# Performance work log

Hardware: AMD Instinct MI355X
Metric: run time of the kernel (lower is better)

## Reference

```python
import jax, jax.numpy as jnp
import numpy as np

B, N, C = 2, 2048, 1024
H = 16
D = C // H  # head_dim = 64
SCALE = D ** -0.5


def setup_inputs() -> dict:
    key = jax.random.key(0)
    ks = jax.random.split(key, 9)
    s = C ** -0.5  # ~ torch Linear default init scale
    return {
        "x": jax.random.normal(ks[0], (B, N, C), dtype=jnp.float32),
        "Wq": jax.random.uniform(ks[1], (C, C), jnp.float32, -s, s),
        "bq": jax.random.uniform(ks[2], (C,), jnp.float32, -s, s),
        "Wk": jax.random.uniform(ks[3], (C, C), jnp.float32, -s, s),
        "bk": jax.random.uniform(ks[4], (C,), jnp.float32, -s, s),
        "Wv": jax.random.uniform(ks[5], (C, C), jnp.float32, -s, s),
        "bv": jax.random.uniform(ks[6], (C,), jnp.float32, -s, s),
        "Wo": jax.random.uniform(ks[7], (C, C), jnp.float32, -s, s),
        "bo": jax.random.uniform(ks[8], (C,), jnp.float32, -s, s),
    }


def reference(x, Wq, bq, Wk, bk, Wv, bv, Wo, bo):
    # Projections: [B,N,C] -> [B,H,N,D]
    def split_heads(t):
        return t.reshape(B, N, H, D).transpose(0, 2, 1, 3)

    q = split_heads(x @ Wq.T + bq)
    k = split_heads(x @ Wk.T + bk)
    v = split_heads(x @ Wv.T + bv)

    scores = jnp.einsum("bhnd,bhmd->bhnm", q, k) * SCALE  # [B,H,N,N]
    attn = jax.nn.softmax(scores, axis=-1)
    out = jnp.einsum("bhnm,bhmd->bhnd", attn, v)  # [B,H,N,D]
    out = out.transpose(0, 2, 1, 3).reshape(B, N, C)
    return out @ Wo.T + bo
```

## Files before the change

kernel.cpp:

```cpp
#include <hip/hip_runtime.h>
#include <stdint.h>


typedef _Float16 h8 __attribute__((ext_vector_type(8)));
typedef _Float16 h4 __attribute__((ext_vector_type(4)));
typedef float f4 __attribute__((ext_vector_type(4)));
typedef uint32_t u32;
typedef u32 u32x4 __attribute__((ext_vector_type(4)));

#define AS1(p) ((const __attribute__((address_space(1))) void*)(p))
#define AS3(p) ((__attribute__((address_space(3))) void*)(p))

template <int ITERS>
__device__ __forceinline__ void stage128B(const _Float16* g, int ldk, _Float16* s, int tid) {
#pragma unroll
  for (int j = 0; j < ITERS; ++j) {
    int off = j * 4096 + tid * 16;
    int row = off >> 7;
    int ch = (off >> 4) & 7;
    int gch = ch ^ (row & 7);
    __builtin_amdgcn_global_load_lds(AS1(g + row * ldk + gch * 8), AS3(s + (off >> 1)), 16, 0, 0);
  }
}

__device__ __forceinline__ void stage_k(const _Float16* g, _Float16* s, int tid) {
#pragma unroll
  for (int j = 0; j < 4; ++j) {
    int off = j * 4096 + tid * 16;
    int row = off >> 7;
    int ch = (off >> 4) & 7;
    int gch = ch ^ ((row >> 1) & 7);
    __builtin_amdgcn_global_load_lds(AS1(g + row * 64 + gch * 8), AS3(s + (off >> 1)), 16, 0, 0);
  }
}

__device__ __forceinline__ void stage_vt(const _Float16* g, _Float16* s, int tid) {
#pragma unroll
  for (int j = 0; j < 4; ++j) {
    int off = j * 4096 + tid * 16;
    int row = off >> 8;
    int ch = (off >> 4) & 15;
    int gch = ch ^ (row & 15);
    __builtin_amdgcn_global_load_lds(AS1(g + row * 2048 + gch * 8), AS3(s + (off >> 1)), 16, 0, 0);
  }
}

__device__ __forceinline__ h8 frag64(const _Float16* s, int row, int g) {
  return *(const h8*)(s + row * 64 + ((g ^ (row & 7)) << 3));
}
__device__ __forceinline__ h8 frag128(const _Float16* s, int row, int g) {
  return *(const h8*)(s + row * 128 + ((g ^ (row & 15)) << 3));
}

__global__ void cvt_all(const float* __restrict__ x, const float* __restrict__ Wq,
                        const float* __restrict__ Wk, const float* __restrict__ Wv,
                        const float* __restrict__ Wo, _Float16* __restrict__ xh,
                        _Float16* __restrict__ q, _Float16* __restrict__ k,
                        _Float16* __restrict__ v, _Float16* __restrict__ o) {
  int blk = blockIdx.x;
  const float* src; _Float16* dst; int off;
  if (blk < 4096)      { src = x;  dst = xh; off = blk; }
  else if (blk < 5120) { src = Wq; dst = q;  off = blk - 4096; }
  else if (blk < 6144) { src = Wk; dst = k;  off = blk - 5120; }
  else if (blk < 7168) { src = Wv; dst = v;  off = blk - 6144; }
  else                 { src = Wo; dst = o;  off = blk - 7168; }
  int i = off * 1024 + threadIdx.x * 4;
  f4 vv = *(const f4*)(src + i);
  h4 ov;
  ov[0] = (_Float16)vv[0]; ov[1] = (_Float16)vv[1]; ov[2] = (_Float16)vv[2]; ov[3] = (_Float16)vv[3];
  *(h4*)(dst + i) = ov;
}

__global__ __launch_bounds__(256, 2) void gemm_qkv(
    const _Float16* __restrict__ X,
    const _Float16* __restrict__ W0, const _Float16* __restrict__ W1, const _Float16* __restrict__ W2,
    const float* __restrict__ b0, const float* __restrict__ b1, const float* __restrict__ b2,
    _Float16* __restrict__ O0, _Float16* __restrict__ O1, _Float16* __restrict__ O2) {
  __shared__ _Float16 As[128 * 64];
  __shared__ _Float16 Bs[128 * 64];
  int z = blockIdx.z;
  const _Float16* W = (z == 0) ? W0 : (z == 1) ? W1 : W2;
  const float* bias = (z == 0) ? b0 : (z == 1) ? b1 : b2;

  int tid = threadIdx.x;
  int lane = tid & 63, wave = tid >> 6;
  int quad = lane >> 4, l15 = lane & 15;
  int wm = (wave >> 1) << 6, wn = (wave & 1) << 6;
  int m0 = blockIdx.y << 7, n0 = blockIdx.x << 7;

  f4 acc[4][4] = {};
  for (int k0 = 0; k0 < 1024; k0 += 64) {
    stage128B<4>(X + m0 * 1024 + k0, 1024, As, tid);
    stage128B<4>(W + n0 * 1024 + k0, 1024, Bs, tid);
    __syncthreads();
#pragma unroll
    for (int ks = 0; ks < 2; ++ks) {
      h8 af[4], bf[4];
#pragma unroll
      for (int i = 0; i < 4; ++i) af[i] = frag64(As, wm + i * 16 + l15, ks * 4 + quad);
#pragma unroll
      for (int i = 0; i < 4; ++i) bf[i] = frag64(Bs, wn + i * 16 + l15, ks * 4 + quad);
#pragma unroll
      for (int mi = 0; mi < 4; ++mi)
#pragma unroll
        for (int ni = 0; ni < 4; ++ni)
          acc[mi][ni] = __builtin_amdgcn_mfma_f32_16x16x32_f16(af[mi], bf[ni], acc[mi][ni], 0, 0, 0);
    }
    __syncthreads();
  }

  if (z == 2) {
#pragma unroll
    for (int mi = 0; mi < 4; ++mi) {
#pragma unroll
      for (int ni = 0; ni < 4; ++ni) {
        int o = n0 + wn + ni * 16 + l15;
        float bv = bias[o];
        int h = o >> 6, dd = o & 63;
        int m = m0 + wm + mi * 16 + quad * 4;
        int b = m >> 11, n = m & 2047;
        h4 v;
#pragma unroll
        for (int r = 0; r < 4; ++r) v[r] = (_Float16)(acc[mi][ni][r] + bv);
        *(h4*)(O2 + (((b * 16 + h) * 64 + dd) * 2048 + n)) = v;
      }
    }
  } else {
    float scale = (z == 0) ? 0.125f * 1.44269504089f : 1.0f;
    _Float16* Out = (z == 0) ? O0 : O1;
#pragma unroll
    for (int mi = 0; mi < 4; ++mi) {
#pragma unroll
      for (int ni = 0; ni < 4; ++ni) {
        int o = n0 + wn + ni * 16 + l15;
        float bv = bias[o];
        int h = o >> 6, d = o & 63;
#pragma unroll
        for (int r = 0; r < 4; ++r) {
          int m = m0 + wm + mi * 16 + quad * 4 + r;
          int b = m >> 11, n = m & 2047;
          float v = (acc[mi][ni][r] + bv) * scale;
          Out[(((b * 16 + h) * 2048 + n) << 6) + d] = (_Float16)v;
        }
      }
    }
  }
}

__global__ __launch_bounds__(256, 2) void gemm_out(
    const _Float16* __restrict__ A, const _Float16* __restrict__ W,
    const float* __restrict__ bias, float* __restrict__ Out) {
  __shared__ _Float16 As[128 * 64];
  __shared__ _Float16 Bs[64 * 64];
  int tid = threadIdx.x;
  int lane = tid & 63, wave = tid >> 6;
  int quad = lane >> 4, l15 = lane & 15;
  int wm = (wave >> 1) << 6, wn = (wave & 1) << 5;
  int m0 = blockIdx.y << 7, n0 = blockIdx.x << 6;

  f4 acc[4][2] = {};
  for (int k0 = 0; k0 < 1024; k0 += 64) {
    stage128B<4>(A + m0 * 1024 + k0, 1024, As, tid);
    stage128B<2>(W + n0 * 1024 + k0, 1024, Bs, tid);
    __syncthreads();
#pragma unroll
    for (int ks = 0; ks < 2; ++ks) {
      h8 af[4], bf[2];
#pragma unroll
      for (int i = 0; i < 4; ++i) af[i] = frag64(As, wm + i * 16 + l15, ks * 4 + quad);
#pragma unroll
      for (int i = 0; i < 2; ++i) bf[i] = frag64(Bs, wn + i * 16 + l15, ks * 4 + quad);
#pragma unroll
      for (int mi = 0; mi < 4; ++mi)
#pragma unroll
        for (int ni = 0; ni < 2; ++ni)
          acc[mi][ni] = __builtin_amdgcn_mfma_f32_16x16x32_f16(af[mi], bf[ni], acc[mi][ni], 0, 0, 0);
    }
    __syncthreads();
  }
#pragma unroll
  for (int mi = 0; mi < 4; ++mi) {
#pragma unroll
    for (int ni = 0; ni < 2; ++ni) {
      int o = n0 + wn + ni * 16 + l15;
      float bv = bias[o];
#pragma unroll
      for (int r = 0; r < 4; ++r) {
        int m = m0 + wm + mi * 16 + quad * 4 + r;
        Out[m * 1024 + o] = acc[mi][ni][r] + bv;
      }
    }
  }
}

__global__ __launch_bounds__(256, 2) void attn(
    const _Float16* __restrict__ Q, const _Float16* __restrict__ Kv,
    const _Float16* __restrict__ Vt, _Float16* __restrict__ AO) {
  __shared__ _Float16 Ks[2][128 * 64];
  __shared__ _Float16 Vs[2][64 * 128];
  int tid = threadIdx.x, lane = tid & 63, wave = tid >> 6;
  int quad = lane >> 4, l15 = lane & 15;
  int bh = blockIdx.y, q0 = blockIdx.x << 7;

  h8 qf[2][2];
#pragma unroll
  for (int s = 0; s < 2; ++s) {
    const _Float16* Qb = Q + (bh * 2048 + q0 + wave * 32 + s * 16) * 64;
#pragma unroll
    for (int ks = 0; ks < 2; ++ks)
      qf[s][ks] = *(const h8*)(Qb + l15 * 64 + ks * 32 + quad * 8);
  }

  const _Float16* Kb = Kv + bh * 131072;
  const _Float16* Vb = Vt + bh * 131072;
  f4 oacc[2][4] = {};
  float lsum[2] = {0.f, 0.f};
  int prow_l = ((l15 >> 2) << 3) + ((l15 & 3) << 1);
  int mask7 = l15 & 7;

  stage_k(Kb, Ks[0], tid);
  stage_vt(Vb, Vs[0], tid);

  for (int kt = 0; kt < 16; ++kt) {
    int cur = kt & 1;
    __syncthreads();
    if (kt < 15) {
      stage_k(Kb + (kt + 1) * 128 * 64, Ks[cur ^ 1], tid);
      stage_vt(Vb + (kt + 1) * 128, Vs[cur ^ 1], tid);
    }
    const _Float16* Kst = Ks[cur];
    const _Float16* Vst = Vs[cur];

    f4 sacc[2][8] = {};
#pragma unroll
    for (int ks = 0; ks < 2; ++ks) {
      int chunk = (ks * 4 + quad) ^ mask7;
#pragma unroll
      for (int ni = 0; ni < 8; ++ni) {
        int prow = ((ni >> 1) << 5) + (ni & 1) + prow_l;
        h8 kf = *(const h8*)(Kst + prow * 64 + chunk * 8);
        sacc[0][ni] = __builtin_amdgcn_mfma_f32_16x16x32_f16(kf, qf[0][ks], sacc[0][ni], 0, 0, 0);
        sacc[1][ni] = __builtin_amdgcn_mfma_f32_16x16x32_f16(kf, qf[1][ks], sacc[1][ni], 0, 0, 0);
      }
    }

    u32 pkw[2][16];
#pragma unroll
    for (int s = 0; s < 2; ++s) {
      float sum = 0.f;
#pragma unroll
      for (int t = 0; t < 4; ++t) {
#pragma unroll
        for (int r = 0; r < 4; ++r) {
          float pa = __builtin_amdgcn_exp2f(sacc[s][2 * t][r]);
          float pb = __builtin_amdgcn_exp2f(sacc[s][2 * t + 1][r]);
          sum += pa + pb;
          pkw[s][t * 4 + r] = __builtin_bit_cast(u32, __builtin_amdgcn_cvt_pkrtz(pa, pb));
        }
      }
      lsum[s] += sum;
    }

#pragma unroll
    for (int t = 0; t < 4; ++t) {
      h8 vf[4];
#pragma unroll
      for (int nd = 0; nd < 4; ++nd) vf[nd] = frag128(Vst, nd * 16 + l15, t * 4 + quad);
#pragma unroll
      for (int s = 0; s < 2; ++s) {
        u32x4 pw = {pkw[s][4 * t + 0], pkw[s][4 * t + 1], pkw[s][4 * t + 2], pkw[s][4 * t + 3]};
        h8 pb = __builtin_bit_cast(h8, pw);
#pragma unroll
        for (int nd = 0; nd < 4; ++nd)
          oacc[s][nd] = __builtin_amdgcn_mfma_f32_16x16x32_f16(vf[nd], pb, oacc[s][nd], 0, 0, 0);
      }
    }
  }

  int b = bh >> 4, h = bh & 15;
#pragma unroll
  for (int s = 0; s < 2; ++s) {
    float l = lsum[s];
    l += __shfl_xor(l, 16);
    l += __shfl_xor(l, 32);
    float inv = 1.0f / l;
    int n = q0 + wave * 32 + s * 16 + l15;
    _Float16* base = AO + (b * 2048 + n) * 1024 + h * 64;
#pragma unroll
    for (int nd = 0; nd < 4; ++nd) {
      h4 o;
#pragma unroll
      for (int r = 0; r < 4; ++r) o[r] = (_Float16)(oacc[s][nd][r] * inv);
      *(h4*)(base + nd * 16 + quad * 4) = o;
    }
  }
}

extern "C" void kernel_launch(void* const* d_in, const int* in_sizes, int n_in,
                              void* d_out, int out_size, void* d_ws, size_t ws_size,
                              hipStream_t stream) {
  const float* x = (const float*)d_in[0];
  const float* Wq = (const float*)d_in[1];
  const float* bq = (const float*)d_in[2];
  const float* Wk = (const float*)d_in[3];
  const float* bk = (const float*)d_in[4];
  const float* Wv = (const float*)d_in[5];
  const float* bv = (const float*)d_in[6];
  const float* Wo = (const float*)d_in[7];
  const float* bo = (const float*)d_in[8];
  float* out = (float*)d_out;

  char* w = (char*)d_ws;
  _Float16* xh  = (_Float16*)(w);
  _Float16* Wqh = (_Float16*)(w + (8u << 20));
  _Float16* Wkh = (_Float16*)(w + (10u << 20));
  _Float16* Wvh = (_Float16*)(w + (12u << 20));
  _Float16* Woh = (_Float16*)(w + (14u << 20));
  _Float16* Qh  = (_Float16*)(w + (16u << 20));
  _Float16* Kh  = (_Float16*)(w + (24u << 20));
  _Float16* Vth = (_Float16*)(w + (32u << 20));
  _Float16* AOh = xh;

  cvt_all<<<8192, 256, 0, stream>>>(x, Wq, Wk, Wv, Wo, xh, Wqh, Wkh, Wvh, Woh);
  gemm_qkv<<<dim3(8, 32, 3), 256, 0, stream>>>(xh, Wqh, Wkh, Wvh, bq, bk, bv, Qh, Kh, Vth);
  attn<<<dim3(16, 32), 256, 0, stream>>>(Qh, Kh, Vth, AOh);
  gemm_out<<<dim3(16, 32), 256, 0, stream>>>(AOh, Woh, bo, out);
}
```

Measured before the change: 179.9 us.

## Switch attention to 32x32x16 MFMA tiles and raise GEMM occupancy hint

The attention kernel is rewritten to use 32x32x16 MFMA instructions in place of 16x16x32. That changes the Q fragment layout, the swizzled K/V LDS read patterns, the exp/pack layout of P, and the output write mapping. K staging now reuses the generic 128-byte swizzled stager. The aim is fewer MFMA issues and fewer LDS fragment loads per tile, at the cost of 16-float accumulators and more register pressure. The QKV and output GEMMs also raise their launch_bounds minimum blocks from 2 to 3, which may force register spilling.

```diff
diff --git a/kernel.cpp b/kernel.cpp
--- a/kernel.cpp
+++ b/kernel.cpp
@@ -5,6 +5,7 @@
 typedef _Float16 h8 __attribute__((ext_vector_type(8)));
 typedef _Float16 h4 __attribute__((ext_vector_type(4)));
 typedef float f4 __attribute__((ext_vector_type(4)));
+typedef float f16f __attribute__((ext_vector_type(16)));
 typedef uint32_t u32;
 typedef u32 u32x4 __attribute__((ext_vector_type(4)));
 
@@ -23,17 +24,6 @@
   }
 }
 
-__device__ __forceinline__ void stage_k(const _Float16* g, _Float16* s, int tid) {
-#pragma unroll
-  for (int j = 0; j < 4; ++j) {
-    int off = j * 4096 + tid * 16;
-    int row = off >> 7;
-    int ch = (off >> 4) & 7;
-    int gch = ch ^ ((row >> 1) & 7);
-    __builtin_amdgcn_global_load_lds(AS1(g + row * 64 + gch * 8), AS3(s + (off >> 1)), 16, 0, 0);
-  }
-}
-
 __device__ __forceinline__ void stage_vt(const _Float16* g, _Float16* s, int tid) {
 #pragma unroll
   for (int j = 0; j < 4; ++j) {
@@ -47,9 +37,6 @@
 
 __device__ __forceinline__ h8 frag64(const _Float16* s, int row, int g) {
   return *(const h8*)(s + row * 64 + ((g ^ (row & 7)) << 3));
-}
-__device__ __forceinline__ h8 frag128(const _Float16* s, int row, int g) {
-  return *(const h8*)(s + row * 128 + ((g ^ (row & 15)) << 3));
 }
 
 __global__ void cvt_all(const float* __restrict__ x, const float* __restrict__ Wq,
@@ -71,7 +58,7 @@
   *(h4*)(dst + i) = ov;
 }
 
-__global__ __launch_bounds__(256, 2) void gemm_qkv(
+__global__ __launch_bounds__(256, 3) void gemm_qkv(
     const _Float16* __restrict__ X,
     const _Float16* __restrict__ W0, const _Float16* __restrict__ W1, const _Float16* __restrict__ W2,
     const float* __restrict__ b0, const float* __restrict__ b1, const float* __restrict__ b2,
@@ -147,7 +134,7 @@
   }
 }
 
-__global__ __launch_bounds__(256, 2) void gemm_out(
+__global__ __launch_bounds__(256, 3) void gemm_out(
     const _Float16* __restrict__ A, const _Float16* __restrict__ W,
     const float* __restrict__ bias, float* __restrict__ Out) {
   __shared__ _Float16 As[128 * 64];
@@ -199,99 +186,89 @@
   __shared__ _Float16 Ks[2][128 * 64];
   __shared__ _Float16 Vs[2][64 * 128];
   int tid = threadIdx.x, lane = tid & 63, wave = tid >> 6;
-  int quad = lane >> 4, l15 = lane & 15;
+  int h = lane >> 5, l31 = lane & 31;
   int bh = blockIdx.y, q0 = blockIdx.x << 7;
 
-  h8 qf[2][2];
-#pragma unroll
-  for (int s = 0; s < 2; ++s) {
-    const _Float16* Qb = Q + (bh * 2048 + q0 + wave * 32 + s * 16) * 64;
-#pragma unroll
-    for (int ks = 0; ks < 2; ++ks)
-      qf[s][ks] = *(const h8*)(Qb + l15 * 64 + ks * 32 + quad * 8);
-  }
+  const _Float16* Qb = Q + (bh * 2048 + q0 + wave * 32 + l31) * 64;
+  h8 qf[4];
+#pragma unroll
+  for (int ks4 = 0; ks4 < 4; ++ks4)
+    qf[ks4] = *(const h8*)(Qb + ks4 * 16 + h * 8);
+
+  int krow = (l31 & 19) | ((l31 & 4) << 1) | ((l31 & 8) >> 1);
+  int kch = krow & 7;
+  int vch = l31 & 15;
 
   const _Float16* Kb = Kv + bh * 131072;
   const _Float16* Vb = Vt + bh * 131072;
-  f4 oacc[2][4] = {};
-  float lsum[2] = {0.f, 0.f};
-  int prow_l = ((l15 >> 2) << 3) + ((l15 & 3) << 1);
-  int mask7 = l15 & 7;
-
-  stage_k(Kb, Ks[0], tid);
+  f16f oacc[2] = {};
+  float lsum = 0.f;
+
+  stage128B<4>(Kb, 64, Ks[0], tid);
   stage_vt(Vb, Vs[0], tid);
 
   for (int kt = 0; kt < 16; ++kt) {
     int cur = kt & 1;
     __syncthreads();
     if (kt < 15) {
-      stage_k(Kb + (kt + 1) * 128 * 64, Ks[cur ^ 1], tid);
+      stage128B<4>(Kb + (kt + 1) * 8192, 64, Ks[cur ^ 1], tid);
       stage_vt(Vb + (kt + 1) * 128, Vs[cur ^ 1], tid);
     }
     const _Float16* Kst = Ks[cur];
     const _Float16* Vst = Vs[cur];
 
-    f4 sacc[2][8] = {};
-#pragma unroll
-    for (int ks = 0; ks < 2; ++ks) {
-      int chunk = (ks * 4 + quad) ^ mask7;
-#pragma unroll
-      for (int ni = 0; ni < 8; ++ni) {
-        int prow = ((ni >> 1) << 5) + (ni & 1) + prow_l;
-        h8 kf = *(const h8*)(Kst + prow * 64 + chunk * 8);
-        sacc[0][ni] = __builtin_amdgcn_mfma_f32_16x16x32_f16(kf, qf[0][ks], sacc[0][ni], 0, 0, 0);
-        sacc[1][ni] = __builtin_amdgcn_mfma_f32_16x16x32_f16(kf, qf[1][ks], sacc[1][ni], 0, 0, 0);
-      }
-    }
-
-    u32 pkw[2][16];
-#pragma unroll
-    for (int s = 0; s < 2; ++s) {
-      float sum = 0.f;
-#pragma unroll
-      for (int t = 0; t < 4; ++t) {
-#pragma unroll
-        for (int r = 0; r < 4; ++r) {
-          float pa = __builtin_amdgcn_exp2f(sacc[s][2 * t][r]);
-          float pb = __builtin_amdgcn_exp2f(sacc[s][2 * t + 1][r]);
-          sum += pa + pb;
-          pkw[s][t * 4 + r] = __builtin_bit_cast(u32, __builtin_amdgcn_cvt_pkrtz(pa, pb));
+    f16f sacc[4] = {};
+#pragma unroll
+    for (int ks4 = 0; ks4 < 4; ++ks4) {
+      int pch = ((ks4 * 2 + h) ^ kch) << 3;
+#pragma unroll
+      for (int kt2 = 0; kt2 < 4; ++kt2) {
+        h8 kf = *(const h8*)(Kst + kt2 * 2048 + krow * 64 + pch);
+        sacc[kt2] = __builtin_amdgcn_mfma_f32_32x32x16_f16(kf, qf[ks4], sacc[kt2], 0, 0, 0);
+      }
+    }
+
+    u32 pkw[4][8];
+#pragma unroll
+    for (int g = 0; g < 4; ++g) {
+#pragma unroll
+      for (int i = 0; i < 8; ++i) {
+        float pa = __builtin_amdgcn_exp2f(sacc[g][2 * i]);
+        float pb = __builtin_amdgcn_exp2f(sacc[g][2 * i + 1]);
+        lsum += pa + pb;
+        pkw[g][i] = __builtin_bit_cast(u32, __builtin_amdgcn_cvt_pkrtz(pa, pb));
+      }
+    }
+
+#pragma unroll
+    for (int g = 0; g < 4; ++g) {
+#pragma unroll
+      for (int s = 0; s < 2; ++s) {
+        u32x4 pw = {pkw[g][4 * s], pkw[g][4 * s + 1], pkw[g][4 * s + 2], pkw[g][4 * s + 3]};
+        h8 pb = __builtin_bit_cast(h8, pw);
+        int ch = ((g * 4 + s * 2 + h) ^ vch) << 3;
+#pragma unroll
+        for (int dt = 0; dt < 2; ++dt) {
+          h8 vf = *(const h8*)(Vst + (dt * 32 + l31) * 128 + ch);
+          oacc[dt] = __builtin_amdgcn_mfma_f32_32x32x16_f16(vf, pb, oacc[dt], 0, 0, 0);
         }
       }
-      lsum[s] += sum;
-    }
-
-#pragma unroll
-    for (int t = 0; t < 4; ++t) {
-      h8 vf[4];
-#pragma unroll
-      for (int nd = 0; nd < 4; ++nd) vf[nd] = frag128(Vst, nd * 16 + l15, t * 4 + quad);
-#pragma unroll
-      for (int s = 0; s < 2; ++s) {
-        u32x4 pw = {pkw[s][4 * t + 0], pkw[s][4 * t + 1], pkw[s][4 * t + 2], pkw[s][4 * t + 3]};
-        h8 pb = __builtin_bit_cast(h8, pw);
-#pragma unroll
-        for (int nd = 0; nd < 4; ++nd)
-          oacc[s][nd] = __builtin_amdgcn_mfma_f32_16x16x32_f16(vf[nd], pb, oacc[s][nd], 0, 0, 0);
-      }
-    }
-  }
-
-  int b = bh >> 4, h = bh & 15;
-#pragma unroll
-  for (int s = 0; s < 2; ++s) {
-    float l = lsum[s];
-    l += __shfl_xor(l, 16);
-    l += __shfl_xor(l, 32);
-    float inv = 1.0f / l;
-    int n = q0 + wave * 32 + s * 16 + l15;
-    _Float16* base = AO + (b * 2048 + n) * 1024 + h * 64;
-#pragma unroll
-    for (int nd = 0; nd < 4; ++nd) {
+    }
+  }
+
+  float l = lsum + __shfl_xor(lsum, 32);
+  float inv = 1.0f / l;
+  int b = bh >> 4, hh = bh & 15;
+  int n = q0 + wave * 32 + l31;
+  _Float16* base = AO + (b * 2048 + n) * 1024 + hh * 64;
+#pragma unroll
+  for (int dt = 0; dt < 2; ++dt) {
+#pragma unroll
+    for (int b2 = 0; b2 < 4; ++b2) {
       h4 o;
 #pragma unroll
-      for (int r = 0; r < 4; ++r) o[r] = (_Float16)(oacc[s][nd][r] * inv);
-      *(h4*)(base + nd * 16 + quad * 4) = o;
+      for (int a = 0; a < 4; ++a) o[a] = (_Float16)(oacc[dt][b2 * 4 + a] * inv);
+      *(h4*)(base + dt * 32 + b2 * 8 + h * 4) = o;
     }
   }
 }
```

Result: no change. 179.7 us (-0.1%).
